# Optimization experiments

Hardware: AMD Instinct MI355X
Metric: run time of the kernel (lower is better)

## Reference

```python
import jax, jax.numpy as jnp
import numpy as np

N_NODES = 50000
N_EDGES = 800000
IN_FEATS, OUT_FEATS, RANK = 256, 128, 64


def setup_inputs() -> dict:
    key = jax.random.key(0)
    ks = jax.random.split(key, 6)
    # xavier-uniform-ish params
    def xavier(k, shape):
        lim = float(np.sqrt(6.0 / (shape[0] + shape[1])))
        return jax.random.uniform(k, shape, jnp.float32, -lim, lim)
    return {
        "feat": jax.random.normal(ks[0], (N_NODES, IN_FEATS), jnp.float32),
        "w1": xavier(ks[1], (IN_FEATS, OUT_FEATS)),
        "w2": xavier(ks[2], (IN_FEATS + 1, RANK)),
        "v": xavier(ks[3], (RANK, OUT_FEATS)),
        "src": jax.random.randint(ks[4], (N_EDGES,), 0, N_NODES, jnp.int32),
        "dst": jax.random.randint(ks[5], (N_EDGES,), 0, N_NODES, jnp.int32),
    }


def reference(feat, w1, w2, v, src, dst):
    n = feat.shape[0]
    ones_e = jnp.ones(src.shape[0], dtype=feat.dtype)
    out_deg = jax.ops.segment_sum(ones_e, src, num_segments=n)  # [N]
    in_deg = jax.ops.segment_sum(ones_e, dst, num_segments=n)   # [N]

    # norm == 'both': scale source features by out_deg^-1/2 (clamped at 1)
    feat_src = feat * (jnp.clip(out_deg, 1.0, None) ** -0.5)[:, None]

    feat_sum = feat_src @ w1  # [N, out_feats]
    feat_prod = jnp.tanh(
        jnp.concatenate([feat_src, jnp.ones((n, 1), feat.dtype)], axis=1) @ w2
    )  # [N, rank]

    # sum-reduce of source messages onto dst (zero for 0-in-degree nodes)
    h_sum = jax.ops.segment_sum(feat_sum[src], dst, num_segments=n)

    # product-reduce via sign/log decomposition (tanh outputs are nonzero a.s.)
    m = feat_prod[src]  # [E, rank]
    log_abs = jax.ops.segment_sum(jnp.log(jnp.abs(m)), dst, num_segments=n)
    neg_cnt = jax.ops.segment_sum((m < 0).astype(jnp.int32), dst, num_segments=n)
    sign = (1 - 2 * (neg_cnt % 2)).astype(feat.dtype)
    # DGL leaves dst nodes with no messages at zero
    h_prod = jnp.where(in_deg[:, None] > 0, sign * jnp.exp(log_abs), 0.0)

    rst = h_sum + h_prod @ v
    # norm == 'both' on destination side: in_deg^-1/2 (clamped at 1)
    rst = rst * (jnp.clip(in_deg, 1.0, None) ** -0.5)[:, None]
    return rst
```

## Files before the change

### kernel.cpp

```cpp
#include <hip/hip_runtime.h>
#include <math.h>

#define N_NODES 50000
#define N_EDGES 800000
#define IN_F 256
#define OUT_F 128
#define RANK 64
#define NCOMB 192
#define REC 192
#define NB_SCAN ((N_NODES + 255) / 256)
#define NB_GEMM ((N_NODES + 63) / 64)
#define NB_H 64
#define CHUNK (N_EDGES / NB_H)
#define HWORDS ((N_NODES + 1) / 2)

typedef unsigned int uint;
typedef unsigned short ushort;
using f32x4 = __attribute__((ext_vector_type(4))) float;
typedef __attribute__((ext_vector_type(8))) short short8;

__device__ __forceinline__ ushort f2bf(float x) {
    uint u = __float_as_uint(x);
    uint r = (u + 0x7fffu + ((u >> 16) & 1u)) >> 16;
    return (ushort)r;
}
__device__ __forceinline__ float bflo(uint u) { return __uint_as_float(u << 16); }
__device__ __forceinline__ float bfhi(uint u) { return __uint_as_float(u & 0xffff0000u); }
__device__ __forceinline__ uint pack2(float lo, float hi) {
    return (uint)f2bf(lo) | ((uint)f2bf(hi) << 16);
}

__global__ __launch_bounds__(256) void k_hist(const float* __restrict__ w1,
                                              const float* __restrict__ w2,
                                              const int* __restrict__ src,
                                              const int* __restrict__ dst,
                                              ushort* __restrict__ BtG,
                                              float* __restrict__ bias,
                                              uint* __restrict__ PIN,
                                              uint* __restrict__ POUT,
                                              ushort* __restrict__ lrank) {
    __shared__ uint hist[HWORDS];
    int b = blockIdx.x;
    int t = threadIdx.x;
    int g = b * 256 + t;

    for (int i = g; i < NCOMB * IN_F; i += 2 * NB_H * 256) {
        int n = i >> 8;
        int k = i & 255;
        float v = (n < OUT_F) ? w1[k * OUT_F + n] : w2[k * RANK + (n - OUT_F)];
        BtG[n * IN_F + k] = f2bf(v);
    }
    if (g < RANK) bias[g] = w2[IN_F * RANK + g];

    for (int w = t; w < HWORDS; w += 256) hist[w] = 0;
    __syncthreads();

    if (b < NB_H) {
        int e0 = b * CHUNK;
        for (int i = t; i < CHUNK / 4; i += 256) {
            int e = e0 + i * 4;
            int4 d4 = *(const int4*)(dst + e);
            uint o0 = atomicAdd(&hist[d4.x >> 1], 1u << ((d4.x & 1) * 16));
            uint o1 = atomicAdd(&hist[d4.y >> 1], 1u << ((d4.y & 1) * 16));
            uint o2 = atomicAdd(&hist[d4.z >> 1], 1u << ((d4.z & 1) * 16));
            uint o3 = atomicAdd(&hist[d4.w >> 1], 1u << ((d4.w & 1) * 16));
            uint r0 = (o0 >> ((d4.x & 1) * 16)) & 0xffffu;
            uint r1 = (o1 >> ((d4.y & 1) * 16)) & 0xffffu;
            uint r2 = (o2 >> ((d4.z & 1) * 16)) & 0xffffu;
            uint r3 = (o3 >> ((d4.w & 1) * 16)) & 0xffffu;
            uint2 pk;
            pk.x = r0 | (r1 << 16);
            pk.y = r2 | (r3 << 16);
            *(uint2*)(lrank + e) = pk;
        }
        __syncthreads();
        for (int w = t; w < HWORDS; w += 256)
            PIN[(size_t)b * HWORDS + w] = hist[w];
    } else {
        int c = b - NB_H;
        int e0 = c * CHUNK;
        for (int i = t; i < CHUNK / 4; i += 256) {
            int e = e0 + i * 4;
            int4 s4 = *(const int4*)(src + e);
            atomicAdd(&hist[s4.x >> 1], 1u << ((s4.x & 1) * 16));
            atomicAdd(&hist[s4.y >> 1], 1u << ((s4.y & 1) * 16));
            atomicAdd(&hist[s4.z >> 1], 1u << ((s4.z & 1) * 16));
            atomicAdd(&hist[s4.w >> 1], 1u << ((s4.w & 1) * 16));
        }
        __syncthreads();
        for (int w = t; w < HWORDS; w += 256)
            POUT[(size_t)c * HWORDS + w] = hist[w];
    }
}

__global__ __launch_bounds__(256) void k_nodescan(const uint* __restrict__ PIN,
                                                  const uint* __restrict__ POUT,
                                                  uint* __restrict__ BPRE,
                                                  int* __restrict__ in_deg,
                                                  int* __restrict__ out_deg) {
    int w = blockIdx.x * 256 + threadIdx.x;
    if (w >= HWORDS) return;
    uint rl = 0, rh = 0;
    for (int b = 0; b < NB_H; ++b) {
        uint v = PIN[(size_t)b * HWORDS + w];
        BPRE[(size_t)b * HWORDS + w] = rl | (rh << 16);
        rl += v & 0xffffu;
        rh += v >> 16;
    }
    in_deg[2 * w] = (int)rl;
    in_deg[2 * w + 1] = (int)rh;
    uint sl = 0, sh = 0;
    for (int b = 0; b < NB_H; ++b) {
        uint v = POUT[(size_t)b * HWORDS + w];
        sl += v & 0xffffu;
        sh += v >> 16;
    }
    out_deg[2 * w] = (int)sl;
    out_deg[2 * w + 1] = (int)sh;
}

__global__ __launch_bounds__(256) void k_bsum(const int* __restrict__ in_deg,
                                              int* __restrict__ bsum) {
    __shared__ int red[4];
    int t = threadIdx.x;
    int idx = blockIdx.x * 256 + t;
    int v = (idx < N_NODES) ? in_deg[idx] : 0;
#pragma unroll
    for (int m = 1; m < 64; m <<= 1) v += __shfl_xor(v, m, 64);
    if ((t & 63) == 0) red[t >> 6] = v;
    __syncthreads();
    if (t == 0) bsum[blockIdx.x] = red[0] + red[1] + red[2] + red[3];
}

__global__ __launch_bounds__(256) void k_scat2(const int* __restrict__ in_deg,
                                               const int* __restrict__ bsum,
                                               int* __restrict__ row_start) {
    __shared__ int s[256];
    int t = threadIdx.x;
    int b = blockIdx.x;
    int bv = (t < NB_SCAN) ? bsum[t] : 0;
    s[t] = bv;
    __syncthreads();
    for (int st = 1; st < 256; st <<= 1) {
        int x = 0;
        if (t >= st) x = s[t - st];
        __syncthreads();
        if (t >= st) s[t] += x;
        __syncthreads();
    }
    int off = (b > 0) ? s[b - 1] : 0;
    __syncthreads();
    int idx = b * 256 + t;
    int v = (idx < N_NODES) ? in_deg[idx] : 0;
    s[t] = v;
    __syncthreads();
    for (int st = 1; st < 256; st <<= 1) {
        int x = 0;
        if (t >= st) x = s[t - st];
        __syncthreads();
        if (t >= st) s[t] += x;
        __syncthreads();
    }
    if (idx < N_NODES) row_start[idx] = off + s[t] - v;
    if (b == NB_SCAN - 1 && t == 0) row_start[N_NODES] = N_EDGES;
}

#define BM 64
#define BK 64
__global__ __launch_bounds__(256) void k_gemmfill(
    const float* __restrict__ feat,
    const ushort* __restrict__ BtG,
    const float* __restrict__ bias,
    const int* __restrict__ out_deg,
    const int* __restrict__ src,
    const int* __restrict__ dst,
    const ushort* __restrict__ lrank,
    const uint* __restrict__ BPRE,
    const int* __restrict__ row_start,
    int* __restrict__ csr_src,
    ushort* __restrict__ feat_rec) {
    __shared__ __align__(16) ushort A_l[BM * BK];
    __shared__ __align__(16) ushort B_l[NCOMB * BK];
    int bid = blockIdx.x;
    int tid = threadIdx.x;

    if (bid & 1) {
        int base = (bid >> 1) * 1024 + tid * 4;
        if (base < N_EDGES) {
            int c = base / CHUNK;
            const uint* bp = BPRE + (size_t)c * HWORDS;
            int4 s4 = *(const int4*)(src + base);
            int4 d4 = *(const int4*)(dst + base);
            uint2 rq = *(const uint2*)(lrank + base);
            int p0 = row_start[d4.x] +
                     (int)((bp[d4.x >> 1] >> ((d4.x & 1) * 16)) & 0xffffu) +
                     (int)(rq.x & 0xffffu);
            int p1 = row_start[d4.y] +
                     (int)((bp[d4.y >> 1] >> ((d4.y & 1) * 16)) & 0xffffu) +
                     (int)(rq.x >> 16);
            int p2 = row_start[d4.z] +
                     (int)((bp[d4.z >> 1] >> ((d4.z & 1) * 16)) & 0xffffu) +
                     (int)(rq.y & 0xffffu);
            int p3 = row_start[d4.w] +
                     (int)((bp[d4.w >> 1] >> ((d4.w & 1) * 16)) & 0xffffu) +
                     (int)(rq.y >> 16);
            csr_src[p0] = s4.x;
            csr_src[p1] = s4.y;
            csr_src[p2] = s4.z;
            csr_src[p3] = s4.w;
        }
        return;
    }

    int gid = bid >> 1;
    int wid = tid >> 6, lane = tid & 63;
    int n0 = gid * BM;

    f32x4 acc[12];
#pragma unroll
    for (int t = 0; t < 12; ++t) acc[t] = (f32x4)(0.f);

    int ar = tid >> 2;
    int ac = (tid & 3) << 4;
    const float* arow = feat + (size_t)(n0 + ar) * IN_F + ac;
    bool arow_ok = (n0 + ar) < N_NODES;

    float4 v0, v1, v2, v3;
    uint4 bg0, bg1, bg2, bg3, bg4, bg5;

#define LOADA(KT)                                                     \
    do {                                                              \
        if (arow_ok) {                                                \
            const float4* p = (const float4*)(arow + (KT) * BK);      \
            v0 = p[0]; v1 = p[1]; v2 = p[2]; v3 = p[3];               \
        } else {                                                      \
            v0 = v1 = v2 = v3 = make_float4(0.f, 0.f, 0.f, 0.f);     \
        }                                                             \
    } while (0)

#define LOADB1(II, DEST)                                              \
    do {                                                              \
        int cc = tid + 256 * (II);                                    \
        int row = cc >> 3;                                            \
        int cb = (cc & 7) << 4;                                       \
        DEST = *(const uint4*)((const char*)BtG + row * 512 + ktn * 128 + cb); \
    } while (0)

    {
        int ktn = 0;
        LOADA(0);
        LOADB1(0, bg0); LOADB1(1, bg1); LOADB1(2, bg2);
        LOADB1(3, bg3); LOADB1(4, bg4); LOADB1(5, bg5);
    }

    for (int kt = 0; kt < 4; ++kt) {
        {
            uint4 w0 = make_uint4(pack2(v0.x, v0.y), pack2(v0.z, v0.w),
                                  pack2(v1.x, v1.y), pack2(v1.z, v1.w));
            uint4 w1q = make_uint4(pack2(v2.x, v2.y), pack2(v2.z, v2.w),
                                   pack2(v3.x, v3.y), pack2(v3.z, v3.w));
            int base = ar * 128 + ac * 2;
            int swz = (ar & 7) << 4;
            *(uint4*)((char*)A_l + (base ^ swz)) = w0;
            *(uint4*)((char*)A_l + ((base + 16) ^ swz)) = w1q;
        }
        {
            uint4 bgs[6] = {bg0, bg1, bg2, bg3, bg4, bg5};
#pragma unroll
            for (int ii = 0; ii < 6; ++ii) {
                int cc = tid + 256 * ii;
                int row = cc >> 3;
                int cb = (cc & 7) << 4;
                int b = (row * 128 + cb) ^ ((row & 7) << 4);
                *(uint4*)((char*)B_l + b) = bgs[ii];
            }
        }
        __syncthreads();
        if (kt < 3) {
            int ktn = kt + 1;
            LOADA(ktn);
            LOADB1(0, bg0); LOADB1(1, bg1); LOADB1(2, bg2);
            LOADB1(3, bg3); LOADB1(4, bg4); LOADB1(5, bg5);
        }
        {
            int arow_f = wid * 16 + (lane & 15);
            int kchunk = lane >> 4;
            int aswz = (arow_f & 7) << 4;
#pragma unroll
            for (int s = 0; s < 2; ++s) {
                int abyte = (arow_f * 128 + s * 64 + kchunk * 16) ^ aswz;
                short8 afrag = *(const short8*)((const char*)A_l + abyte);
#pragma unroll
                for (int t = 0; t < 12; ++t) {
                    int brow = t * 16 + (lane & 15);
                    int bbyte = (brow * 128 + s * 64 + kchunk * 16) ^ ((brow & 7) << 4);
                    short8 bfrag = *(const short8*)((const char*)B_l + bbyte);
                    acc[t] = __builtin_amdgcn_mfma_f32_16x16x32_bf16(afrag, bfrag,
                                                                     acc[t], 0, 0, 0);
                }
            }
        }
        __syncthreads();
    }

    int col = lane & 15;
    int r0 = wid * 16 + ((lane >> 4) << 2);
#pragma unroll
    for (int q = 0; q < 4; ++q) {
        int n = n0 + r0 + q;
        if (n < N_NODES) {
            float s = rsqrtf(fmaxf((float)out_deg[n], 1.f));
            ushort* rec = feat_rec + (size_t)n * REC;
#pragma unroll
            for (int t = 0; t < 8; ++t)
                rec[t * 16 + col] = f2bf(acc[t][q] * s);
#pragma unroll
            for (int t = 8; t < 12; ++t) {
                float z = acc[t][q] * s + bias[(t - 8) * 16 + col];
                rec[OUT_F + (t - 8) * 16 + col] = f2bf(tanhf(z));
            }
        }
    }
}

__global__ __launch_bounds__(256) void k_agg(const ushort* __restrict__ feat_rec,
                                             const int* __restrict__ row_start,
                                             const int* __restrict__ csr_src,
                                             const float* __restrict__ vmat,
                                             float* __restrict__ out) {
    __shared__ float sum_s[4][OUT_F];
    __shared__ float prod_s[4][RANK];
    int wid = threadIdx.x >> 6;
    int lane = threadIdx.x & 63;
    int g = lane >> 4;
    int i = lane & 15;
    int d = blockIdx.x * 4 + wid;

    int beg = row_start[d];
    int end = row_start[d + 1];
    int deg = end - beg;

    const char* frb = (const char*)feat_rec;

    float a0 = 0.f, a1 = 0.f, a2 = 0.f, a3 = 0.f;
    float a4 = 0.f, a5 = 0.f, a6 = 0.f, a7 = 0.f;
    float p0 = 1.f, p1 = 1.f, p2 = 1.f, p3 = 1.f;

    if (deg > 0) {
        int cl = end - 1;
        int e0 = beg + g * 4;
        int sA = csr_src[min(e0 + 0, cl)];
        int sB = csr_src[min(e0 + 1, cl)];
        int sC = csr_src[min(e0 + 2, cl)];
        int sD = csr_src[min(e0 + 3, cl)];
        int niter = (deg + 15) >> 4;
        for (int it = 0; it < niter; ++it) {
            size_t bA = (size_t)sA * 384, bB = (size_t)sB * 384;
            size_t bC = (size_t)sC * 384, bD = (size_t)sD * 384;
            uint4 uA = *(const uint4*)(frb + bA + (i << 4));
            uint4 uB = *(const uint4*)(frb + bB + (i << 4));
            uint4 uC = *(const uint4*)(frb + bC + (i << 4));
            uint4 uD = *(const uint4*)(frb + bD + (i << 4));
            uint2 qA = *(const uint2*)(frb + bA + 256 + (i << 3));
            uint2 qB = *(const uint2*)(frb + bB + 256 + (i << 3));
            uint2 qC = *(const uint2*)(frb + bC + 256 + (i << 3));
            uint2 qD = *(const uint2*)(frb + bD + 256 + (i << 3));
            bool vA = (e0 + 0) < end;
            bool vB = (e0 + 1) < end;
            bool vC = (e0 + 2) < end;
            bool vD = (e0 + 3) < end;
            float mA = vA ? 1.f : 0.f;
            float mB = vB ? 1.f : 0.f;
            float mC = vC ? 1.f : 0.f;
            float mD = vD ? 1.f : 0.f;
            e0 += 16;
            sA = csr_src[min(e0 + 0, cl)];
            sB = csr_src[min(e0 + 1, cl)];
            sC = csr_src[min(e0 + 2, cl)];
            sD = csr_src[min(e0 + 3, cl)];
            a0 = fmaf(mA, bflo(uA.x), a0); a1 = fmaf(mA, bfhi(uA.x), a1);
            a2 = fmaf(mA, bflo(uA.y), a2); a3 = fmaf(mA, bfhi(uA.y), a3);
            a4 = fmaf(mA, bflo(uA.z), a4); a5 = fmaf(mA, bfhi(uA.z), a5);
            a6 = fmaf(mA, bflo(uA.w), a6); a7 = fmaf(mA, bfhi(uA.w), a7);
            a0 = fmaf(mB, bflo(uB.x), a0); a1 = fmaf(mB, bfhi(uB.x), a1);
            a2 = fmaf(mB, bflo(uB.y), a2); a3 = fmaf(mB, bfhi(uB.y), a3);
            a4 = fmaf(mB, bflo(uB.z), a4); a5 = fmaf(mB, bfhi(uB.z), a5);
            a6 = fmaf(mB, bflo(uB.w), a6); a7 = fmaf(mB, bfhi(uB.w), a7);
            a0 = fmaf(mC, bflo(uC.x), a0); a1 = fmaf(mC, bfhi(uC.x), a1);
            a2 = fmaf(mC, bflo(uC.y), a2); a3 = fmaf(mC, bfhi(uC.y), a3);
            a4 = fmaf(mC, bflo(uC.z), a4); a5 = fmaf(mC, bfhi(uC.z), a5);
            a6 = fmaf(mC, bflo(uC.w), a6); a7 = fmaf(mC, bfhi(uC.w), a7);
            a0 = fmaf(mD, bflo(uD.x), a0); a1 = fmaf(mD, bfhi(uD.x), a1);
            a2 = fmaf(mD, bflo(uD.y), a2); a3 = fmaf(mD, bfhi(uD.y), a3);
            a4 = fmaf(mD, bflo(uD.z), a4); a5 = fmaf(mD, bfhi(uD.z), a5);
            a6 = fmaf(mD, bflo(uD.w), a6); a7 = fmaf(mD, bfhi(uD.w), a7);
            p0 *= vA ? bflo(qA.x) : 1.f; p1 *= vA ? bfhi(qA.x) : 1.f;
            p2 *= vA ? bflo(qA.y) : 1.f; p3 *= vA ? bfhi(qA.y) : 1.f;
            p0 *= vB ? bflo(qB.x) : 1.f; p1 *= vB ? bfhi(qB.x) : 1.f;
            p2 *= vB ? bflo(qB.y) : 1.f; p3 *= vB ? bfhi(qB.y) : 1.f;
            p0 *= vC ? bflo(qC.x) : 1.f; p1 *= vC ? bfhi(qC.x) : 1.f;
            p2 *= vC ? bflo(qC.y) : 1.f; p3 *= vC ? bfhi(qC.y) : 1.f;
            p0 *= vD ? bflo(qD.x) : 1.f; p1 *= vD ? bfhi(qD.x) : 1.f;
            p2 *= vD ? bflo(qD.y) : 1.f; p3 *= vD ? bfhi(qD.y) : 1.f;
        }
    }

    a0 += __shfl_xor(a0, 16, 64); a0 += __shfl_xor(a0, 32, 64);
    a1 += __shfl_xor(a1, 16, 64); a1 += __shfl_xor(a1, 32, 64);
    a2 += __shfl_xor(a2, 16, 64); a2 += __shfl_xor(a2, 32, 64);
    a3 += __shfl_xor(a3, 16, 64); a3 += __shfl_xor(a3, 32, 64);
    a4 += __shfl_xor(a4, 16, 64); a4 += __shfl_xor(a4, 32, 64);
    a5 += __shfl_xor(a5, 16, 64); a5 += __shfl_xor(a5, 32, 64);
    a6 += __shfl_xor(a6, 16, 64); a6 += __shfl_xor(a6, 32, 64);
    a7 += __shfl_xor(a7, 16, 64); a7 += __shfl_xor(a7, 32, 64);
    p0 *= __shfl_xor(p0, 16, 64); p0 *= __shfl_xor(p0, 32, 64);
    p1 *= __shfl_xor(p1, 16, 64); p1 *= __shfl_xor(p1, 32, 64);
    p2 *= __shfl_xor(p2, 16, 64); p2 *= __shfl_xor(p2, 32, 64);
    p3 *= __shfl_xor(p3, 16, 64); p3 *= __shfl_xor(p3, 32, 64);

    if (g == 0) {
        sum_s[wid][i * 8 + 0] = a0; sum_s[wid][i * 8 + 1] = a1;
        sum_s[wid][i * 8 + 2] = a2; sum_s[wid][i * 8 + 3] = a3;
        sum_s[wid][i * 8 + 4] = a4; sum_s[wid][i * 8 + 5] = a5;
        sum_s[wid][i * 8 + 6] = a6; sum_s[wid][i * 8 + 7] = a7;
        prod_s[wid][i * 4 + 0] = p0; prod_s[wid][i * 4 + 1] = p1;
        prod_s[wid][i * 4 + 2] = p2; prod_s[wid][i * 4 + 3] = p3;
    }

    float o0 = sum_s[wid][lane * 2];
    float o1 = sum_s[wid][lane * 2 + 1];
    if (deg > 0) {
#pragma unroll 8
        for (int r = 0; r < RANK; ++r) {
            float p = prod_s[wid][r];
            float2 v2 = *(const float2*)(vmat + r * OUT_F + lane * 2);
            o0 += p * v2.x;
            o1 += p * v2.y;
        }
    }
    float sc = rsqrtf(fmaxf((float)deg, 1.f));
    float2 res;
    res.x = o0 * sc;
    res.y = o1 * sc;
    *(float2*)(out + (size_t)d * OUT_F + lane * 2) = res;
}

extern "C" void kernel_launch(void* const* d_in, const int* in_sizes, int n_in,
                              void* d_out, int out_size, void* d_ws, size_t ws_size,
                              hipStream_t stream) {
    const float* feat = (const float*)d_in[0];
    const float* w1   = (const float*)d_in[1];
    const float* w2   = (const float*)d_in[2];
    const float* vmat = (const float*)d_in[3];
    const int*   src  = (const int*)d_in[4];
    const int*   dst  = (const int*)d_in[5];
    float* out = (float*)d_out;

    char* ws = (char*)d_ws;
    size_t off = 0;
    auto alloc = [&](size_t bytes) {
        void* p = ws + off;
        off = (off + bytes + 255) & ~(size_t)255;
        return p;
    };
    int* out_deg   = (int*)alloc(N_NODES * sizeof(int));
    int* in_deg    = (int*)alloc(N_NODES * sizeof(int));
    int* row_start = (int*)alloc((N_NODES + 1) * sizeof(int));
    int* csr_src   = (int*)alloc(N_EDGES * sizeof(int));
    int* bsum      = (int*)alloc(NB_SCAN * sizeof(int));
    uint* PIN      = (uint*)alloc((size_t)NB_H * HWORDS * sizeof(uint));
    uint* POUT     = (uint*)alloc((size_t)NB_H * HWORDS * sizeof(uint));
    uint* BPRE     = (uint*)alloc((size_t)NB_H * HWORDS * sizeof(uint));
    ushort* lrank  = (ushort*)alloc(N_EDGES * sizeof(ushort));
    ushort* feat_rec = (ushort*)alloc((size_t)N_NODES * REC * sizeof(ushort));
    ushort* BtG      = (ushort*)alloc((size_t)NCOMB * IN_F * sizeof(ushort));
    float*  bias     = (float*)alloc(RANK * sizeof(float));

    k_hist<<<2 * NB_H, 256, 0, stream>>>(w1, w2, src, dst, BtG, bias,
                                         PIN, POUT, lrank);
    k_nodescan<<<(HWORDS + 255) / 256, 256, 0, stream>>>(PIN, POUT, BPRE,
                                                         in_deg, out_deg);
    k_bsum<<<NB_SCAN, 256, 0, stream>>>(in_deg, bsum);
    k_scat2<<<NB_SCAN, 256, 0, stream>>>(in_deg, bsum, row_start);
    k_gemmfill<<<NB_GEMM * 2, 256, 0, stream>>>(feat, BtG, bias, out_deg,
                                                src, dst, lrank, BPRE, row_start,
                                                csr_src, feat_rec);
    k_agg<<<N_NODES / 4, 256, 0, stream>>>(feat_rec, row_start, csr_src,
                                           vmat, out);
}
```

Before: 178.8 us.

## Raise histogram block count and fold block-sum reduction into node scan

Raises the number of edge-histogram chunks from 64 to 125, so the histogram launch uses 250 blocks and fills more compute units on the first pass. Removes the separate k_bsum kernel by computing per-256-node block sums inside k_nodescan with a shared-memory tree reduction, saving one launch and one reread of in_deg. In exchange, the per-chunk partial histogram arrays (PIN, POUT, BPRE) roughly double in size. The node scan now loops serially over 125 chunks instead of 64, which adds memory traffic and latency to that kernel.

```diff
diff --git a/kernel.cpp b/kernel.cpp
--- a/kernel.cpp
+++ b/kernel.cpp
@@ -10,7 +10,7 @@
 #define REC 192
 #define NB_SCAN ((N_NODES + 255) / 256)
 #define NB_GEMM ((N_NODES + 63) / 64)
-#define NB_H 64
+#define NB_H 125
 #define CHUNK (N_EDGES / NB_H)
 #define HWORDS ((N_NODES + 1) / 2)
 
@@ -97,39 +97,38 @@
                                                   const uint* __restrict__ POUT,
                                                   uint* __restrict__ BPRE,
                                                   int* __restrict__ in_deg,
-                                                  int* __restrict__ out_deg) {
-    int w = blockIdx.x * 256 + threadIdx.x;
-    if (w >= HWORDS) return;
+                                                  int* __restrict__ out_deg,
+                                                  int* __restrict__ bsum) {
+    __shared__ int sr[256];
+    int t = threadIdx.x;
+    int b = blockIdx.x;
+    int w = b * 256 + t;
     uint rl = 0, rh = 0;
-    for (int b = 0; b < NB_H; ++b) {
-        uint v = PIN[(size_t)b * HWORDS + w];
-        BPRE[(size_t)b * HWORDS + w] = rl | (rh << 16);
-        rl += v & 0xffffu;
-        rh += v >> 16;
-    }
-    in_deg[2 * w] = (int)rl;
-    in_deg[2 * w + 1] = (int)rh;
-    uint sl = 0, sh = 0;
-    for (int b = 0; b < NB_H; ++b) {
-        uint v = POUT[(size_t)b * HWORDS + w];
-        sl += v & 0xffffu;
-        sh += v >> 16;
-    }
-    out_deg[2 * w] = (int)sl;
-    out_deg[2 * w + 1] = (int)sh;
-}
-
-__global__ __launch_bounds__(256) void k_bsum(const int* __restrict__ in_deg,
-                                              int* __restrict__ bsum) {
-    __shared__ int red[4];
-    int t = threadIdx.x;
-    int idx = blockIdx.x * 256 + t;
-    int v = (idx < N_NODES) ? in_deg[idx] : 0;
-#pragma unroll
-    for (int m = 1; m < 64; m <<= 1) v += __shfl_xor(v, m, 64);
-    if ((t & 63) == 0) red[t >> 6] = v;
+    if (w < HWORDS) {
+        for (int c = 0; c < NB_H; ++c) {
+            uint v = PIN[(size_t)c * HWORDS + w];
+            BPRE[(size_t)c * HWORDS + w] = rl | (rh << 16);
+            rl += v & 0xffffu;
+            rh += v >> 16;
+        }
+        in_deg[2 * w] = (int)rl;
+        in_deg[2 * w + 1] = (int)rh;
+        uint sl = 0, sh = 0;
+        for (int c = 0; c < NB_H; ++c) {
+            uint v = POUT[(size_t)c * HWORDS + w];
+            sl += v & 0xffffu;
+            sh += v >> 16;
+        }
+        out_deg[2 * w] = (int)sl;
+        out_deg[2 * w + 1] = (int)sh;
+    }
+    sr[t] = (int)(rl + rh);
     __syncthreads();
-    if (t == 0) bsum[blockIdx.x] = red[0] + red[1] + red[2] + red[3];
+    for (int st = 64; st > 0; st >>= 1) {
+        if ((t & 127) < st) sr[t] += sr[t + st];
+        __syncthreads();
+    }
+    if ((t & 127) == 0) bsum[2 * b + (t >> 7)] = sr[t];
 }
 
 __global__ __launch_bounds__(256) void k_scat2(const int* __restrict__ in_deg,
@@ -479,8 +478,7 @@
     k_hist<<<2 * NB_H, 256, 0, stream>>>(w1, w2, src, dst, BtG, bias,
                                          PIN, POUT, lrank);
     k_nodescan<<<(HWORDS + 255) / 256, 256, 0, stream>>>(PIN, POUT, BPRE,
-                                                         in_deg, out_deg);
-    k_bsum<<<NB_SCAN, 256, 0, stream>>>(in_deg, bsum);
+                                                         in_deg, out_deg, bsum);
     k_scat2<<<NB_SCAN, 256, 0, stream>>>(in_deg, bsum, row_start);
     k_gemmfill<<<NB_GEMM * 2, 256, 0, stream>>>(feat, BtG, bias, out_deg,
                                                 src, dst, lrank, BPRE, row_start,
```

Result: slower. 192.1 us (+7.4%).
